# Kernel optimization log

Measured on AMD Instinct MI355X. Metric: run time of the kernel, lower is better.

Reference implementation:

```python
import jax, jax.numpy as jnp
import numpy as np

N = 50000      # nodes
E = 800000     # edges (avg degree 16)
DIN = 128
DH = 128
DOUT = 64


def setup_inputs() -> dict:
    key = jax.random.key(0)
    ks = jax.random.split(key, 12)
    s = lambda d: 1.0 / np.sqrt(d)
    return {
        "x":   jax.random.normal(ks[0], (N, DIN), jnp.float32),
        "W1l": jax.random.normal(ks[1], (DIN, DH), jnp.float32) * s(DIN),
        "W1r": jax.random.normal(ks[2], (DIN, DH), jnp.float32) * s(DIN),
        "b1":  jnp.zeros((DH,), jnp.float32),
        "W2l": jax.random.normal(ks[3], (DH, DH), jnp.float32) * s(DH),
        "W2r": jax.random.normal(ks[4], (DH, DH), jnp.float32) * s(DH),
        "b2":  jnp.zeros((DH,), jnp.float32),
        "W3l": jax.random.normal(ks[5], (DH, DOUT), jnp.float32) * s(DH),
        "W3r": jax.random.normal(ks[6], (DH, DOUT), jnp.float32) * s(DH),
        "b3":  jnp.zeros((DOUT,), jnp.float32),
        "src": jax.random.randint(ks[7], (E,), 0, N, dtype=jnp.int32),
        "dst": jax.random.randint(ks[8], (E,), 0, N, dtype=jnp.int32),
    }


def _sage_conv(x, src, dst, Wl, Wr, b):
    """PyG SAGEConv (mean aggr): lin_l(mean_{j in N(i)} x_j) + lin_r(x_i) + b.
    adj_t row = target (dst), col = source (src)."""
    n = x.shape[0]
    agg = jax.ops.segment_sum(x[src], dst, num_segments=n)          # [N, d]
    deg = jax.ops.segment_sum(jnp.ones(src.shape, x.dtype), dst, num_segments=n)
    mean = agg / jnp.maximum(deg, 1.0)[:, None]
    return mean @ Wl + x @ Wr + b


def reference(x, W1l, W1r, b1, W2l, W2r, b2, W3l, W3r, b3, src, dst):
    # dropout uses inference semantics (identity) for a deterministic baseline
    h = jax.nn.elu(_sage_conv(x, src, dst, W1l, W1r, b1))
    h = jax.nn.elu(_sage_conv(h, src, dst, W2l, W2r, b2))
    h = jax.nn.elu(_sage_conv(h, src, dst, W3l, W3r, b3))
    return jax.nn.log_softmax(h, axis=-1)
```

## Files before the change

kernel.cpp:

```cpp
#include <hip/hip_runtime.h>
#include <math.h>

constexpr int FEAT = 128;

typedef __attribute__((ext_vector_type(8))) short short8v;
typedef __attribute__((ext_vector_type(4))) float f32x4;
typedef __attribute__((ext_vector_type(2))) float f32x2;
typedef __attribute__((ext_vector_type(4))) int   int4v;

__device__ inline unsigned short f2bf(float f) {
    unsigned int u = __float_as_uint(f);
    u += 0x7fffu + ((u >> 16) & 1u);
    return (unsigned short)(u >> 16);
}
__device__ inline float bf2f(unsigned short h) {
    return __uint_as_float(((unsigned int)h) << 16);
}
__device__ inline unsigned char f2fp8(float f) {
    int r = __builtin_amdgcn_cvt_pk_fp8_f32(f, 0.f, 0, false);
    return (unsigned char)(r & 0xff);
}

__global__ __launch_bounds__(1024) void bucket_kernel(const int* __restrict__ src,
                                                      const int* __restrict__ dst,
                                                      unsigned int* __restrict__ chunkdata,
                                                      int* __restrict__ table,
                                                      int E, int nb) {
    __shared__ int cnt[128];
    __shared__ int part[128];
    __shared__ int sbase[128];
    __shared__ unsigned int sbuf[8192];
    const int t = threadIdx.x;
    const int c = blockIdx.x;
    const int e0 = c * 8192;

    if (t < 128) cnt[t] = 0;
    __syncthreads();

    unsigned int word[8];
    int bkt[8], rnk[8];
    #pragma unroll
    for (int it = 0; it < 2; ++it) {
        int e = e0 + it * 4096 + t * 4;
        int4 d4 = make_int4(0, 0, 0, 0), s4 = d4;
        if (e + 3 < E) {
            d4 = *(const int4*)(dst + e);
            s4 = *(const int4*)(src + e);
        } else {
            if (e + 0 < E) { d4.x = dst[e + 0]; s4.x = src[e + 0]; } else d4.x = -1;
            if (e + 1 < E) { d4.y = dst[e + 1]; s4.y = src[e + 1]; } else d4.y = -1;
            if (e + 2 < E) { d4.z = dst[e + 2]; s4.z = src[e + 2]; } else d4.z = -1;
            if (e + 3 < E) { d4.w = dst[e + 3]; s4.w = src[e + 3]; } else d4.w = -1;
        }
        int dd[4] = {d4.x, d4.y, d4.z, d4.w};
        int ss[4] = {s4.x, s4.y, s4.z, s4.w};
        #pragma unroll
        for (int q = 0; q < 4; ++q) {
            int i = it * 4 + q;
            int d = dd[q];
            if (d >= 0) {
                bkt[i]  = d >> 9;
                rnk[i]  = atomicAdd(&cnt[bkt[i]], 1);
                word[i] = (unsigned int)ss[q] | ((unsigned int)(d & 511) << 16);
            } else bkt[i] = -1;
        }
    }
    __syncthreads();

    if (t < 128) part[t] = cnt[t];
    __syncthreads();
    for (int s = 1; s < 128; s <<= 1) {
        int v = (t >= s && t < 128) ? part[t - s] : 0;
        __syncthreads();
        if (t < 128) part[t] += v;
        __syncthreads();
    }
    if (t < 128) sbase[t] = part[t] - cnt[t];
    __syncthreads();

    if (t <= nb) table[(size_t)c * (nb + 1) + t] = sbase[t];

    #pragma unroll
    for (int i = 0; i < 8; ++i)
        if (bkt[i] >= 0) sbuf[sbase[bkt[i]] + rnk[i]] = word[i];
    __syncthreads();

    const int total = part[127];
    for (int i = t; i < total; i += 1024)
        chunkdata[(size_t)c * 8192 + i] = sbuf[i];
}

constexpr int P2CAP = 10240;
__global__ __launch_bounds__(1024) void fillsort_kernel(const unsigned int* __restrict__ chunkdata,
                                                        const int* __restrict__ table,
                                                        int* __restrict__ offs,
                                                        float* __restrict__ invd,
                                                        int* __restrict__ eidx,
                                                        int n, int nch, int nbk, int E) {
    __shared__ int cnt[512];
    __shared__ int lcur[512];
    __shared__ int part[512];
    __shared__ int redb[16];
    __shared__ int lbuf[P2CAP];
    const int b  = blockIdx.x;
    const int t  = threadIdx.x;
    const int lo = b << 9;

    int partial = 0;
    for (int c = t; c < nch; c += 1024) partial += table[(size_t)c * (nbk + 1) + b];
    #pragma unroll
    for (int off = 32; off > 0; off >>= 1) partial += __shfl_down(partial, off, 64);
    if ((t & 63) == 0) redb[t >> 6] = partial;
    for (int i = t; i < 512; i += 1024) cnt[i] = 0;
    __syncthreads();
    int base = 0;
    #pragma unroll
    for (int i = 0; i < 16; ++i) base += redb[i];

    const int w    = t >> 6;
    const int lane = t & 63;
    for (int c = w; c < nch; c += 16) {
        int o0 = table[(size_t)c * (nbk + 1) + b];
        int o1 = table[(size_t)c * (nbk + 1) + b + 1];
        for (int i = o0 + lane; i < o1; i += 64)
            atomicAdd(&cnt[(chunkdata[(size_t)c * 8192 + i] >> 16) & 511], 1);
    }
    __syncthreads();

    int v = (t < 512) ? cnt[t] : 0;
    if (t < 512) part[t] = v;
    __syncthreads();
    for (int s = 1; s < 512; s <<= 1) {
        int u = (t >= s && t < 512) ? part[t - s] : 0;
        __syncthreads();
        if (t < 512) part[t] += u;
        __syncthreads();
    }
    const int total = part[511];
    if (t < 512) {
        int ex = part[t] - v;
        lcur[t] = ex;
        int idx = lo + t;
        if (idx < n) {
            offs[idx] = base + ex;
            invd[idx] = 1.0f / fmaxf((float)v, 1.0f);
        }
    }
    if (b == nbk - 1 && t == 0) offs[n] = E;
    __syncthreads();

    for (int c = w; c < nch; c += 16) {
        int o0 = table[(size_t)c * (nbk + 1) + b];
        int o1 = table[(size_t)c * (nbk + 1) + b + 1];
        for (int i = o0 + lane; i < o1; i += 64) {
            unsigned int wd = chunkdata[(size_t)c * 8192 + i];
            int s = wd & 0xffff;
            int p = atomicAdd(&lcur[(wd >> 16) & 511], 1);
            if (p < P2CAP) lbuf[p] = s;
            else           eidx[base + p] = s;
        }
    }
    __syncthreads();

    const int m = min(total, P2CAP);
    for (int i = t; i < m; i += 1024) eidx[base + i] = lbuf[i];
}

__global__ void deg_kernel(const int* __restrict__ dst, int* __restrict__ degi, int E) {
    int e = blockIdx.x * 256 + threadIdx.x;
    if (e < E) atomicAdd(&degi[__builtin_nontemporal_load(dst + e)], 1);
}
__global__ __launch_bounds__(256) void blockred_kernel(const int* __restrict__ deg,
                                                       int* __restrict__ bsum, int n) {
    __shared__ int red[256];
    int base = blockIdx.x * 1024 + threadIdx.x * 4;
    int s = 0;
    if (base + 3 < n) {
        int4 v = *(const int4*)(deg + base);
        s = v.x + v.y + v.z + v.w;
    } else {
        for (int i = 0; i < 4; ++i) if (base + i < n) s += deg[base + i];
    }
    red[threadIdx.x] = s;
    __syncthreads();
    for (int st = 128; st > 0; st >>= 1) {
        if (threadIdx.x < st) red[threadIdx.x] += red[threadIdx.x + st];
        __syncthreads();
    }
    if (threadIdx.x == 0) bsum[blockIdx.x] = red[0];
}
__global__ __launch_bounds__(256) void scanb_kernel(const int* __restrict__ bsum,
                                                    int* __restrict__ bpre, int nb) {
    __shared__ int part[256];
    int t = threadIdx.x;
    int v = (t < nb) ? bsum[t] : 0;
    part[t] = v;
    __syncthreads();
    for (int s = 1; s < 256; s <<= 1) {
        int u = (t >= s) ? part[t - s] : 0;
        __syncthreads();
        part[t] += u;
        __syncthreads();
    }
    if (t < nb) bpre[t] = part[t] - v;
}
__global__ __launch_bounds__(256) void scanfill_kernel(const int* __restrict__ deg,
                                                       const int* __restrict__ bpre,
                                                       int* __restrict__ offs,
                                                       int* __restrict__ cur,
                                                       float* __restrict__ invd,
                                                       int n, int E) {
    __shared__ int part[256];
    int t = threadIdx.x;
    int base = blockIdx.x * 1024 + t * 4;
    int d[4];
    int s = 0;
    #pragma unroll
    for (int i = 0; i < 4; ++i) {
        d[i] = (base + i < n) ? deg[base + i] : 0;
        s += d[i];
    }
    part[t] = s;
    __syncthreads();
    for (int st = 1; st < 256; st <<= 1) {
        int u = (t >= st) ? part[t - st] : 0;
        __syncthreads();
        part[t] += u;
        __syncthreads();
    }
    int pre = bpre[blockIdx.x] + part[t] - s;
    #pragma unroll
    for (int i = 0; i < 4; ++i) {
        int idx = base + i;
        if (idx < n) {
            offs[idx] = pre;
            cur[idx]  = pre;
            invd[idx] = 1.0f / fmaxf((float)d[i], 1.0f);
            pre += d[i];
        }
    }
    if (blockIdx.x == 0 && t == 0) offs[n] = E;
}
constexpr int FCH = 4096;
__global__ __launch_bounds__(256) void fill_xcd_kernel(const int* __restrict__ src,
                                                       const int* __restrict__ dst,
                                                       int* __restrict__ cur,
                                                       int* __restrict__ eidx,
                                                       int E, int rsize) {
    const int p     = blockIdx.x & 7;
    const int chunk = blockIdx.x >> 3;
    const int lo = p * rsize;
    const int hi = lo + rsize;
    #pragma unroll
    for (int it = 0; it < 4; ++it) {
        int e = chunk * FCH + (it * 256 + threadIdx.x) * 4;
        if (e + 3 < E) {
            int4v d4 = __builtin_nontemporal_load((const int4v*)(dst + e));
            #pragma unroll
            for (int q = 0; q < 4; ++q) {
                int d = d4[q];
                if (d >= lo && d < hi) {
                    int pos = atomicAdd(&cur[d], 1);
                    eidx[pos] = __builtin_nontemporal_load(src + e + q);
                }
            }
        } else {
            for (int q = 0; e + q < E && q < 4; ++q) {
                int d = dst[e + q];
                if (d >= lo && d < hi) {
                    int pos = atomicAdd(&cur[d], 1);
                    eidx[pos] = src[e + q];
                }
            }
        }
    }
}

__global__ __launch_bounds__(256) void prep_kernel(
    const float* __restrict__ W1l, const float* __restrict__ W1r,
    const float* __restrict__ W2l, const float* __restrict__ W2r,
    const float* __restrict__ W3l, const float* __restrict__ W3r,
    unsigned short* __restrict__ WTh1, unsigned short* __restrict__ WTl1,
    unsigned short* __restrict__ WTh2, unsigned short* __restrict__ WTl2,
    unsigned short* __restrict__ WTh3, unsigned short* __restrict__ WTl3,
    const float* __restrict__ x, unsigned short* __restrict__ xbf,
    unsigned char* __restrict__ xf8, int total4)
{
    const int b = blockIdx.x;
    if (b < 320) {
        const float *Wl, *Wr;
        unsigned short *WTh, *WTl;
        int dout, idx;
        if (b < 128)      { Wl = W1l; Wr = W1r; WTh = WTh1; WTl = WTl1; dout = 128; idx = b * 256 + threadIdx.x; }
        else if (b < 256) { Wl = W2l; Wr = W2r; WTh = WTh2; WTl = WTl2; dout = 128; idx = (b - 128) * 256 + threadIdx.x; }
        else              { Wl = W3l; Wr = W3r; WTh = WTh3; WTl = WTl3; dout = 64;  idx = (b - 256) * 256 + threadIdx.x; }
        if (idx < dout * 256) {
            int c = idx >> 8;
            int k = idx & 255;
            float v = (k < 128) ? Wl[(size_t)k * dout + c] : Wr[(size_t)(k - 128) * dout + c];
            unsigned short h = f2bf(v);
            WTh[(size_t)c * 256 + k] = h;
            WTl[(size_t)c * 256 + k] = f2bf(v - bf2f(h));
        }
    } else {
        int i = (b - 320) * 256 + threadIdx.x;
        if (i < total4) {
            float4 v = *(const float4*)(x + (size_t)i * 4);
            ushort4 h;
            h.x = f2bf(v.x); h.y = f2bf(v.y); h.z = f2bf(v.z); h.w = f2bf(v.w);
            *(ushort4*)(xbf + (size_t)i * 4) = h;
            uchar4 c;
            c.x = f2fp8(v.x); c.y = f2fp8(v.y); c.z = f2fp8(v.z); c.w = f2fp8(v.w);
            *(uchar4*)(xf8 + (size_t)i * 4) = c;
        }
    }
}

__global__ __launch_bounds__(256) void gather_f8_kernel(const unsigned char* __restrict__ featf8,
                                                        const int* __restrict__ offs,
                                                        const int* __restrict__ eidx,
                                                        const float* __restrict__ invd,
                                                        unsigned short* __restrict__ aggbf, int n) {
    int node = blockIdx.x * 4 + (threadIdx.x >> 6);
    if (node >= n) return;
    const int l   = threadIdx.x & 63;
    const int grp = l >> 4;
    const int li  = l & 15;
    const int c8  = li * 8;
    int beg = offs[node], end = offs[node + 1];
    float acc[8];
    #pragma unroll
    for (int q = 0; q < 8; ++q) acc[q] = 0.f;

    int j = beg + grp;
    for (; j + 4 < end; j += 8) {
        int s0 = eidx[j], s1 = eidx[j + 4];
        uint2 v0 = *(const uint2*)(featf8 + (size_t)s0 * FEAT + c8);
        uint2 v1 = *(const uint2*)(featf8 + (size_t)s1 * FEAT + c8);
        f32x2 p;
        p = __builtin_amdgcn_cvt_pk_f32_fp8(v0.x, false); acc[0] += p.x; acc[1] += p.y;
        p = __builtin_amdgcn_cvt_pk_f32_fp8(v0.x, true);  acc[2] += p.x; acc[3] += p.y;
        p = __builtin_amdgcn_cvt_pk_f32_fp8(v0.y, false); acc[4] += p.x; acc[5] += p.y;
        p = __builtin_amdgcn_cvt_pk_f32_fp8(v0.y, true);  acc[6] += p.x; acc[7] += p.y;
        p = __builtin_amdgcn_cvt_pk_f32_fp8(v1.x, false); acc[0] += p.x; acc[1] += p.y;
        p = __builtin_amdgcn_cvt_pk_f32_fp8(v1.x, true);  acc[2] += p.x; acc[3] += p.y;
        p = __builtin_amdgcn_cvt_pk_f32_fp8(v1.y, false); acc[4] += p.x; acc[5] += p.y;
        p = __builtin_amdgcn_cvt_pk_f32_fp8(v1.y, true);  acc[6] += p.x; acc[7] += p.y;
    }
    if (j < end) {
        int s0 = eidx[j];
        uint2 v0 = *(const uint2*)(featf8 + (size_t)s0 * FEAT + c8);
        f32x2 p;
        p = __builtin_amdgcn_cvt_pk_f32_fp8(v0.x, false); acc[0] += p.x; acc[1] += p.y;
        p = __builtin_amdgcn_cvt_pk_f32_fp8(v0.x, true);  acc[2] += p.x; acc[3] += p.y;
        p = __builtin_amdgcn_cvt_pk_f32_fp8(v0.y, false); acc[4] += p.x; acc[5] += p.y;
        p = __builtin_amdgcn_cvt_pk_f32_fp8(v0.y, true);  acc[6] += p.x; acc[7] += p.y;
    }

    #pragma unroll
    for (int off = 16; off < 64; off <<= 1)
        #pragma unroll
        for (int q = 0; q < 8; ++q)
            acc[q] += __shfl_xor(acc[q], off, 64);

    if (grp == 0) {
        float sc = invd[node];
        unsigned short o[8];
        #pragma unroll
        for (int q = 0; q < 8; ++q) o[q] = f2bf(acc[q] * sc);
        *(short8v*)(aggbf + (size_t)node * FEAT + c8) = *(short8v*)o;
    }
}

template <int DOUT, bool WBF, bool WF8, bool LSM>
__global__ __launch_bounds__(1024, 4) void dense_mfma(
    const unsigned short* __restrict__ meanbf, const unsigned short* __restrict__ xinbf,
    const unsigned short* __restrict__ WTh, const unsigned short* __restrict__ WTl,
    const float* __restrict__ bias,
    float* outf, unsigned short* outbf, unsigned char* outf8, int n)
{
    __shared__ unsigned short Bh[64 * 256];
    __shared__ unsigned short Bl[64 * 256];
    const int tid = threadIdx.x;
    const int colbase = blockIdx.y * 64;

    #pragma unroll
    for (int it = 0; it < 2; ++it) {
        int o  = (tid + it * 1024) * 8;
        int cl = o >> 8;
        int k  = o & 255;
        size_t gsrc = (size_t)(colbase + cl) * 256 + k;
        int db = (o * 2) ^ ((cl & 7) << 4);
        *(short8v*)((char*)Bh + db) = *(const short8v*)(WTh + gsrc);
        *(short8v*)((char*)Bl + db) = *(const short8v*)(WTl + gsrc);
    }
    __syncthreads();

    const int l    = tid & 63;
    const int w    = tid >> 6;
    const int l15  = l & 15;
    const int lg   = l >> 4;
    const int row0 = blockIdx.x * 256 + w * 16;
    if (row0 >= n) return;
    const int g = row0 + l15;

    f32x4 acc[4];
    #pragma unroll
    for (int ct = 0; ct < 4; ++ct) acc[ct] = (f32x4){0.f, 0.f, 0.f, 0.f};

    #pragma unroll
    for (int ch = 0; ch < 8; ++ch) {
        const unsigned short* As = (ch < 4) ? meanbf : xinbf;
        const int kb = (ch & 3) * 32 + lg * 8;
        short8v ah = (short8v){0, 0, 0, 0, 0, 0, 0, 0};
        if (g < n) ah = *(const short8v*)(As + (size_t)g * FEAT + kb);
        #pragma unroll
        for (int ct = 0; ct < 4; ++ct) {
            int cl = ct * 16 + l15;
            int db = (cl * 512 + ch * 64 + lg * 16) ^ ((cl & 7) << 4);
            short8v bh = *(const short8v*)((const char*)Bh + db);
            short8v bl = *(const short8v*)((const char*)Bl + db);
            acc[ct] = __builtin_amdgcn_mfma_f32_16x16x32_bf16(ah, bh, acc[ct], 0, 0, 0);
            acc[ct] = __builtin_amdgcn_mfma_f32_16x16x32_bf16(ah, bl, acc[ct], 0, 0, 0);
        }
    }

    float t[4][4];
    #pragma unroll
    for (int ct = 0; ct < 4; ++ct) {
        float b = bias[colbase + ct * 16 + l15];
        #pragma unroll
        for (int q = 0; q < 4; ++q) {
            float v = acc[ct][q] + b;
            t[ct][q] = (v > 0.f) ? v : expm1f(v);
        }
    }
    if (LSM) {
        #pragma unroll
        for (int q = 0; q < 4; ++q) {
            float m = t[0][q];
            #pragma unroll
            for (int ct = 1; ct < 4; ++ct) m = fmaxf(m, t[ct][q]);
            #pragma unroll
            for (int s = 1; s < 16; s <<= 1) m = fmaxf(m, __shfl_xor(m, s, 64));
            float sum = 0.f;
            #pragma unroll
            for (int ct = 0; ct < 4; ++ct) sum += expf(t[ct][q] - m);
            #pragma unroll
            for (int s = 1; s < 16; s <<= 1) sum += __shfl_xor(sum, s, 64);
            float ls = m + logf(sum);
            #pragma unroll
            for (int ct = 0; ct < 4; ++ct) t[ct][q] -= ls;
        }
    }
    #pragma unroll
    for (int ct = 0; ct < 4; ++ct) {
        int col = colbase + ct * 16 + l15;
        #pragma unroll
        for (int q = 0; q < 4; ++q) {
            int grow = row0 + lg * 4 + q;
            if (grow < n) {
                if (WBF) outbf[(size_t)grow * DOUT + col] = f2bf(t[ct][q]);
                if (WF8) outf8[(size_t)grow * DOUT + col] = f2fp8(t[ct][q]);
                if (!WBF && !WF8) outf[(size_t)grow * DOUT + col] = t[ct][q];
            }
        }
    }
}

extern "C" void kernel_launch(void* const* d_in, const int* in_sizes, int n_in,
                              void* d_out, int out_size, void* d_ws, size_t ws_size,
                              hipStream_t stream) {
    const float* x   = (const float*)d_in[0];
    const float* W1l = (const float*)d_in[1];
    const float* W1r = (const float*)d_in[2];
    const float* b1  = (const float*)d_in[3];
    const float* W2l = (const float*)d_in[4];
    const float* W2r = (const float*)d_in[5];
    const float* b2  = (const float*)d_in[6];
    const float* W3l = (const float*)d_in[7];
    const float* W3r = (const float*)d_in[8];
    const float* b3  = (const float*)d_in[9];
    const int*   src = (const int*)d_in[10];
    const int*   dst = (const int*)d_in[11];

    const int N = in_sizes[0] / FEAT;
    const int E = in_sizes[10];

    const size_t NA = ((size_t)N + 63) & ~(size_t)63;
    const size_t EA = ((size_t)E + 63) & ~(size_t)63;
    const int nb  = (N + 1023) / 1024;
    const int nbk = (N + 511) >> 9;
    const int nch = (E + 8191) / 8192;

    auto alignup = [](char* p) { return (char*)(((uintptr_t)p + 255) & ~(uintptr_t)255); };
    char* p = (char*)d_ws;
    float* invd = (float*)p;                 p += NA * 4;
    int*   offs = (int*)p;                   p += (NA + 64) * 4;
    int*   eidx = (int*)p;                   p += EA * 4;
    unsigned int* chunkd = (unsigned int*)p; p += (size_t)nch * 8192 * 4;
    int*   table = (int*)p;                  p += (size_t)nch * (nbk + 1) * 4;
    p = alignup(p);
    int*   deg  = (int*)p;                   p += NA * 4;
    int*   cur  = (int*)p;                   p += NA * 4;
    int*   bsum = (int*)p;                   p += 256 * 4;
    int*   bpre = (int*)p;                   p += 256 * 4;
    p = alignup(p);
    unsigned short* WTh1 = (unsigned short*)p; p += 128 * 256 * 2;
    unsigned short* WTl1 = (unsigned short*)p; p += 128 * 256 * 2;
    unsigned short* WTh2 = (unsigned short*)p; p += 128 * 256 * 2;
    unsigned short* WTl2 = (unsigned short*)p; p += 128 * 256 * 2;
    unsigned short* WTh3 = (unsigned short*)p; p += 64 * 256 * 2;
    unsigned short* WTl3 = (unsigned short*)p; p += 64 * 256 * 2;
    p = alignup(p);
    unsigned short* mbf = (unsigned short*)p;  p += NA * FEAT * 2;
    unsigned short* bfA = (unsigned short*)p;  p += NA * FEAT * 2;
    unsigned short* bfB = (unsigned short*)p;  p += NA * FEAT * 2;
    unsigned char*  f8X = (unsigned char*)p;   p += NA * FEAT;
    float* outp = (float*)d_out;

    const int gblocks = (N + 3) / 4;
    const int dblocks = (N + 255) / 256;
    const int total4  = N * FEAT / 4;

    if (N <= 65536) {
        bucket_kernel<<<nch, 1024, 0, stream>>>(src, dst, chunkd, table, E, nbk);
        fillsort_kernel<<<nbk, 1024, 0, stream>>>(chunkd, table, offs, invd, eidx, N, nch, nbk, E);
    } else {
        hipMemsetAsync(deg, 0, (size_t)N * 4, stream);
        deg_kernel<<<(E + 255) / 256, 256, 0, stream>>>(dst, deg, E);
        blockred_kernel<<<nb, 256, 0, stream>>>(deg, bsum, N);
        scanb_kernel<<<1, 256, 0, stream>>>(bsum, bpre, nb);
        scanfill_kernel<<<nb, 256, 0, stream>>>(deg, bpre, offs, cur, invd, N, E);
        const int rsize   = (N + 7) / 8;
        const int fblocks = ((E + FCH - 1) / FCH) * 8;
        fill_xcd_kernel<<<fblocks, 256, 0, stream>>>(src, dst, cur, eidx, E, rsize);
    }
    prep_kernel<<<320 + (total4 + 255) / 256, 256, 0, stream>>>(
        W1l, W1r, W2l, W2r, W3l, W3r, WTh1, WTl1, WTh2, WTl2, WTh3, WTl3,
        x, bfA, f8X, total4);

    gather_f8_kernel<<<gblocks, 256, 0, stream>>>(f8X, offs, eidx, invd, mbf, N);
    dense_mfma<128, true, true, false><<<dim3(dblocks, 2), 1024, 0, stream>>>(mbf, bfA, WTh1, WTl1, b1, nullptr, bfB, f8X, N);

    gather_f8_kernel<<<gblocks, 256, 0, stream>>>(f8X, offs, eidx, invd, mbf, N);
    dense_mfma<128, true, true, false><<<dim3(dblocks, 2), 1024, 0, stream>>>(mbf, bfB, WTh2, WTl2, b2, nullptr, bfA, f8X, N);

    gather_f8_kernel<<<gblocks, 256, 0, stream>>>(f8X, offs, eidx, invd, mbf, N);
    dense_mfma<64, false, false, true><<<dim3(dblocks, 1), 1024, 0, stream>>>(mbf, bfA, WTh3, WTl3, b3, outp, nullptr, nullptr, N);
}
```

Measured before the change: 161.1 us.

## Fuse prep into bucket kernel, use 16-bit edge indices, full-width dense tiles

Weight and feature preparation now runs in extra blocks of the bucketing kernel, which removes one launch and lets the two overlap. For small graphs the fill-sort writes edge source indices as 16-bit values, and the gather kernel is templated to read them, which halves index traffic in all three gathers. The dense MFMA kernel now covers every output column in a single block instead of splitting them across blockIdx.y. That avoids reading the activation rows twice, but it needs much more LDS per block (up to 128KB for the 128-wide layers), which can lower occupancy.

```diff
diff --git a/kernel.cpp b/kernel.cpp
--- a/kernel.cpp
+++ b/kernel.cpp
@@ -21,17 +21,59 @@
     return (unsigned char)(r & 0xff);
 }
 
-__global__ __launch_bounds__(1024) void bucket_kernel(const int* __restrict__ src,
-                                                      const int* __restrict__ dst,
-                                                      unsigned int* __restrict__ chunkdata,
-                                                      int* __restrict__ table,
-                                                      int E, int nb) {
+__global__ __launch_bounds__(1024) void bucket_prep_kernel(
+    const int* __restrict__ src, const int* __restrict__ dst,
+    unsigned int* __restrict__ chunkdata, int* __restrict__ table,
+    int E, int nbk, int nch,
+    const float* __restrict__ W1l, const float* __restrict__ W1r,
+    const float* __restrict__ W2l, const float* __restrict__ W2r,
+    const float* __restrict__ W3l, const float* __restrict__ W3r,
+    unsigned short* __restrict__ WTh1, unsigned short* __restrict__ WTl1,
+    unsigned short* __restrict__ WTh2, unsigned short* __restrict__ WTl2,
+    unsigned short* __restrict__ WTh3, unsigned short* __restrict__ WTl3,
+    const float* __restrict__ x, unsigned short* __restrict__ xbf,
+    unsigned char* __restrict__ xf8, int total4)
+{
     __shared__ int cnt[128];
     __shared__ int part[128];
     __shared__ int sbase[128];
     __shared__ unsigned int sbuf[8192];
     const int t = threadIdx.x;
-    const int c = blockIdx.x;
+    const int blk = blockIdx.x;
+
+    if (blk >= nch) {
+        int b = blk - nch;
+        if (b < 80) {
+            const float *Wl, *Wr;
+            unsigned short *WTh, *WTl;
+            int dout, idx;
+            if (b < 32)      { Wl = W1l; Wr = W1r; WTh = WTh1; WTl = WTl1; dout = 128; idx = b * 1024 + t; }
+            else if (b < 64) { Wl = W2l; Wr = W2r; WTh = WTh2; WTl = WTl2; dout = 128; idx = (b - 32) * 1024 + t; }
+            else             { Wl = W3l; Wr = W3r; WTh = WTh3; WTl = WTl3; dout = 64;  idx = (b - 64) * 1024 + t; }
+            if (idx < dout * 256) {
+                int c = idx >> 8;
+                int k = idx & 255;
+                float v = (k < 128) ? Wl[(size_t)k * dout + c] : Wr[(size_t)(k - 128) * dout + c];
+                unsigned short h = f2bf(v);
+                WTh[(size_t)c * 256 + k] = h;
+                WTl[(size_t)c * 256 + k] = f2bf(v - bf2f(h));
+            }
+        } else {
+            int i = (b - 80) * 1024 + t;
+            if (i < total4) {
+                float4 v = *(const float4*)(x + (size_t)i * 4);
+                ushort4 h;
+                h.x = f2bf(v.x); h.y = f2bf(v.y); h.z = f2bf(v.z); h.w = f2bf(v.w);
+                *(ushort4*)(xbf + (size_t)i * 4) = h;
+                uchar4 c;
+                c.x = f2fp8(v.x); c.y = f2fp8(v.y); c.z = f2fp8(v.z); c.w = f2fp8(v.w);
+                *(uchar4*)(xf8 + (size_t)i * 4) = c;
+            }
+        }
+        return;
+    }
+
+    const int c = blk;
     const int e0 = c * 8192;
 
     if (t < 128) cnt[t] = 0;
@@ -78,7 +120,7 @@
     if (t < 128) sbase[t] = part[t] - cnt[t];
     __syncthreads();
 
-    if (t <= nb) table[(size_t)c * (nb + 1) + t] = sbase[t];
+    if (t <= nbk) table[(size_t)c * (nbk + 1) + t] = sbase[t];
 
     #pragma unroll
     for (int i = 0; i < 8; ++i)
@@ -95,7 +137,7 @@
                                                         const int* __restrict__ table,
                                                         int* __restrict__ offs,
                                                         float* __restrict__ invd,
-                                                        int* __restrict__ eidx,
+                                                        unsigned short* __restrict__ eidx,
                                                         int n, int nch, int nbk, int E) {
     __shared__ int cnt[512];
     __shared__ int lcur[512];
@@ -157,13 +199,13 @@
             int s = wd & 0xffff;
             int p = atomicAdd(&lcur[(wd >> 16) & 511], 1);
             if (p < P2CAP) lbuf[p] = s;
-            else           eidx[base + p] = s;
+            else           eidx[base + p] = (unsigned short)s;
         }
     }
     __syncthreads();
 
     const int m = min(total, P2CAP);
-    for (int i = t; i < m; i += 1024) eidx[base + i] = lbuf[i];
+    for (int i = t; i < m; i += 1024) eidx[base + i] = (unsigned short)lbuf[i];
 }
 
 __global__ void deg_kernel(const int* __restrict__ dst, int* __restrict__ degi, int E) {
@@ -275,7 +317,6 @@
         }
     }
 }
-
 __global__ __launch_bounds__(256) void prep_kernel(
     const float* __restrict__ W1l, const float* __restrict__ W1r,
     const float* __restrict__ W2l, const float* __restrict__ W2r,
@@ -316,9 +357,10 @@
     }
 }
 
+template <typename IT>
 __global__ __launch_bounds__(256) void gather_f8_kernel(const unsigned char* __restrict__ featf8,
                                                         const int* __restrict__ offs,
-                                                        const int* __restrict__ eidx,
+                                                        const IT* __restrict__ eidx,
                                                         const float* __restrict__ invd,
                                                         unsigned short* __restrict__ aggbf, int n) {
     int node = blockIdx.x * 4 + (threadIdx.x >> 6);
@@ -379,17 +421,17 @@
     const float* __restrict__ bias,
     float* outf, unsigned short* outbf, unsigned char* outf8, int n)
 {
-    __shared__ unsigned short Bh[64 * 256];
-    __shared__ unsigned short Bl[64 * 256];
+    constexpr int NCT = DOUT / 16;
+    __shared__ unsigned short Bh[DOUT * 256];
+    __shared__ unsigned short Bl[DOUT * 256];
     const int tid = threadIdx.x;
-    const int colbase = blockIdx.y * 64;
-
-    #pragma unroll
-    for (int it = 0; it < 2; ++it) {
+
+    #pragma unroll
+    for (int it = 0; it < DOUT / 32; ++it) {
         int o  = (tid + it * 1024) * 8;
         int cl = o >> 8;
         int k  = o & 255;
-        size_t gsrc = (size_t)(colbase + cl) * 256 + k;
+        size_t gsrc = (size_t)cl * 256 + k;
         int db = (o * 2) ^ ((cl & 7) << 4);
         *(short8v*)((char*)Bh + db) = *(const short8v*)(WTh + gsrc);
         *(short8v*)((char*)Bl + db) = *(const short8v*)(WTl + gsrc);
@@ -404,9 +446,9 @@
     if (row0 >= n) return;
     const int g = row0 + l15;
 
-    f32x4 acc[4];
-    #pragma unroll
-    for (int ct = 0; ct < 4; ++ct) acc[ct] = (f32x4){0.f, 0.f, 0.f, 0.f};
+    f32x4 acc[NCT];
+    #pragma unroll
+    for (int ct = 0; ct < NCT; ++ct) acc[ct] = (f32x4){0.f, 0.f, 0.f, 0.f};
 
     #pragma unroll
     for (int ch = 0; ch < 8; ++ch) {
@@ -415,7 +457,7 @@
         short8v ah = (short8v){0, 0, 0, 0, 0, 0, 0, 0};
         if (g < n) ah = *(const short8v*)(As + (size_t)g * FEAT + kb);
         #pragma unroll
-        for (int ct = 0; ct < 4; ++ct) {
+        for (int ct = 0; ct < NCT; ++ct) {
             int cl = ct * 16 + l15;
             int db = (cl * 512 + ch * 64 + lg * 16) ^ ((cl & 7) << 4);
             short8v bh = *(const short8v*)((const char*)Bh + db);
@@ -425,10 +467,10 @@
         }
     }
 
-    float t[4][4];
-    #pragma unroll
-    for (int ct = 0; ct < 4; ++ct) {
-        float b = bias[colbase + ct * 16 + l15];
+    float t[NCT][4];
+    #pragma unroll
+    for (int ct = 0; ct < NCT; ++ct) {
+        float b = bias[ct * 16 + l15];
         #pragma unroll
         for (int q = 0; q < 4; ++q) {
             float v = acc[ct][q] + b;
@@ -440,22 +482,22 @@
         for (int q = 0; q < 4; ++q) {
             float m = t[0][q];
             #pragma unroll
-            for (int ct = 1; ct < 4; ++ct) m = fmaxf(m, t[ct][q]);
+            for (int ct = 1; ct < NCT; ++ct) m = fmaxf(m, t[ct][q]);
             #pragma unroll
             for (int s = 1; s < 16; s <<= 1) m = fmaxf(m, __shfl_xor(m, s, 64));
             float sum = 0.f;
             #pragma unroll
-            for (int ct = 0; ct < 4; ++ct) sum += expf(t[ct][q] - m);
+            for (int ct = 0; ct < NCT; ++ct) sum += expf(t[ct][q] - m);
             #pragma unroll
             for (int s = 1; s < 16; s <<= 1) sum += __shfl_xor(sum, s, 64);
             float ls = m + logf(sum);
             #pragma unroll
-            for (int ct = 0; ct < 4; ++ct) t[ct][q] -= ls;
-        }
-    }
-    #pragma unroll
-    for (int ct = 0; ct < 4; ++ct) {
-        int col = colbase + ct * 16 + l15;
+            for (int ct = 0; ct < NCT; ++ct) t[ct][q] -= ls;
+        }
+    }
+    #pragma unroll
+    for (int ct = 0; ct < NCT; ++ct) {
+        int col = ct * 16 + l15;
         #pragma unroll
         for (int q = 0; q < 4; ++q) {
             int grow = row0 + lg * 4 + q;
@@ -497,7 +539,8 @@
     char* p = (char*)d_ws;
     float* invd = (float*)p;                 p += NA * 4;
     int*   offs = (int*)p;                   p += (NA + 64) * 4;
-    int*   eidx = (int*)p;                   p += EA * 4;
+    int*   eidxi = (int*)p;                  p += EA * 4;
+    unsigned short* eidx16 = (unsigned short*)eidxi;
     unsigned int* chunkd = (unsigned int*)p; p += (size_t)nch * 8192 * 4;
     int*   table = (int*)p;                  p += (size_t)nch * (nbk + 1) * 4;
     p = alignup(p);
@@ -524,8 +567,22 @@
     const int total4  = N * FEAT / 4;
 
     if (N <= 65536) {
-        bucket_kernel<<<nch, 1024, 0, stream>>>(src, dst, chunkd, table, E, nbk);
-        fillsort_kernel<<<nbk, 1024, 0, stream>>>(chunkd, table, offs, invd, eidx, N, nch, nbk, E);
+        const int pblocks = 80 + (total4 + 1023) / 1024;
+        bucket_prep_kernel<<<nch + pblocks, 1024, 0, stream>>>(
+            src, dst, chunkd, table, E, nbk, nch,
+            W1l, W1r, W2l, W2r, W3l, W3r,
+            WTh1, WTl1, WTh2, WTl2, WTh3, WTl3,
+            x, bfA, f8X, total4);
+        fillsort_kernel<<<nbk, 1024, 0, stream>>>(chunkd, table, offs, invd, eidx16, N, nch, nbk, E);
+
+        gather_f8_kernel<unsigned short><<<gblocks, 256, 0, stream>>>(f8X, offs, eidx16, invd, mbf, N);
+        dense_mfma<128, true, true, false><<<dblocks, 1024, 0, stream>>>(mbf, bfA, WTh1, WTl1, b1, nullptr, bfB, f8X, N);
+
+        gather_f8_kernel<unsigned short><<<gblocks, 256, 0, stream>>>(f8X, offs, eidx16, invd, mbf, N);
+        dense_mfma<128, true, true, false><<<dblocks, 1024, 0, stream>>>(mbf, bfB, WTh2, WTl2, b2, nullptr, bfA, f8X, N);
+
+        gather_f8_kernel<unsigned short><<<gblocks, 256, 0, stream>>>(f8X, offs, eidx16, invd, mbf, N);
+        dense_mfma<64, false, false, true><<<dblocks, 1024, 0, stream>>>(mbf, bfA, WTh3, WTl3, b3, outp, nullptr, nullptr, N);
     } else {
         hipMemsetAsync(deg, 0, (size_t)N * 4, stream);
         deg_kernel<<<(E + 255) / 256, 256, 0, stream>>>(dst, deg, E);
@@ -534,18 +591,18 @@
         scanfill_kernel<<<nb, 256, 0, stream>>>(deg, bpre, offs, cur, invd, N, E);
         const int rsize   = (N + 7) / 8;
         const int fblocks = ((E + FCH - 1) / FCH) * 8;
-        fill_xcd_kernel<<<fblocks, 256, 0, stream>>>(src, dst, cur, eidx, E, rsize);
-    }
-    prep_kernel<<<320 + (total4 + 255) / 256, 256, 0, stream>>>(
-        W1l, W1r, W2l, W2r, W3l, W3r, WTh1, WTl1, WTh2, WTl2, WTh3, WTl3,
-        x, bfA, f8X, total4);
-
-    gather_f8_kernel<<<gblocks, 256, 0, stream>>>(f8X, offs, eidx, invd, mbf, N);
-    dense_mfma<128, true, true, false><<<dim3(dblocks, 2), 1024, 0, stream>>>(mbf, bfA, WTh1, WTl1, b1, nullptr, bfB, f8X, N);
-
-    gather_f8_kernel<<<gblocks, 256, 0, stream>>>(f8X, offs, eidx, invd, mbf, N);
-    dense_mfma<128, true, true, false><<<dim3(dblocks, 2), 1024, 0, stream>>>(mbf, bfB, WTh2, WTl2, b2, nullptr, bfA, f8X, N);
-
-    gather_f8_kernel<<<gblocks, 256, 0, stream>>>(f8X, offs, eidx, invd, mbf, N);
-    dense_mfma<64, false, false, true><<<dim3(dblocks, 1), 1024, 0, stream>>>(mbf, bfA, WTh3, WTl3, b3, outp, nullptr, nullptr, N);
-}
+        fill_xcd_kernel<<<fblocks, 256, 0, stream>>>(src, dst, cur, eidxi, E, rsize);
+        prep_kernel<<<320 + (total4 + 255) / 256, 256, 0, stream>>>(
+            W1l, W1r, W2l, W2r, W3l, W3r, WTh1, WTl1, WTh2, WTl2, WTh3, WTl3,
+            x, bfA, f8X, total4);
+
+        gather_f8_kernel<int><<<gblocks, 256, 0, stream>>>(f8X, offs, eidxi, invd, mbf, N);
+        dense_mfma<128, true, true, false><<<dblocks, 1024, 0, stream>>>(mbf, bfA, WTh1, WTl1, b1, nullptr, bfB, f8X, N);
+
+        gather_f8_kernel<int><<<gblocks, 256, 0, stream>>>(f8X, offs, eidxi, invd, mbf, N);
+        dense_mfma<128, true, true, false><<<dblocks, 1024, 0, stream>>>(mbf, bfB, WTh2, WTl2, b2, nullptr, bfA, f8X, N);
+
+        gather_f8_kernel<int><<<gblocks, 256, 0, stream>>>(f8X, offs, eidxi, invd, mbf, N);
+        dense_mfma<64, false, false, true><<<dblocks, 1024, 0, stream>>>(mbf, bfA, WTh3, WTl3, b3, outp, nullptr, nullptr, N);
+    }
+}
```

Result: no change. 159.6 us (-1.0%).
